# Kernel optimization log

Measured on AMD Instinct MI355X. Metric: run time of the kernel, lower is better.

The kernel has to match this reference:

```python
import jax, jax.numpy as jnp
import numpy as np

L, B, D = 2048, 8, 768
EPS_BN = 1e-5
EPS_LN = 1e-5
SCALE = 1.0 / float(np.sqrt(D))


def setup_inputs() -> dict:
    key = jax.random.key(0)
    ks = jax.random.split(key, 8)
    f32 = jnp.float32
    return {
        "x_a": jax.random.normal(ks[0], (L, B, D), dtype=f32),
        "x_v": jax.random.normal(ks[1], (L, B, D), dtype=f32),
        "x": jax.random.normal(ks[2], (L, B, D), dtype=f32),
        # conv1x1 (audio branch): weight [out_ch, in_ch], bias [out_ch]
        "W_a": jax.random.normal(ks[3], (D, D), dtype=f32) * 0.02,
        "b_a": jnp.zeros((D,), f32),
        "bn_a_g": jnp.ones((D,), f32),
        "bn_a_b": jnp.zeros((D,), f32),
        "prelu_a": jnp.full((1,), 0.25, f32),
        # conv1x1 (video branch)
        "W_v": jax.random.normal(ks[4], (D, D), dtype=f32) * 0.02,
        "b_v": jnp.zeros((D,), f32),
        "bn_v_g": jnp.ones((D,), f32),
        "bn_v_b": jnp.zeros((D,), f32),
        "prelu_v": jnp.full((1,), 0.25, f32),
        # final LayerNorm affine
        "ln_g": jnp.ones((D,), f32),
        "ln_b": jnp.zeros((D,), f32),
    }


def _branch(q, kv, W, b, bn_g, bn_b, alpha):
    # q: [B, L, D] queries; kv: [B, Lm, D] keys == values (cross-modal)
    attn = jax.nn.softmax(jnp.einsum('bld,bmd->blm', q, kv) * SCALE, axis=-1)
    ctx = jnp.einsum('blm,bmd->bld', attn, kv)            # [B, L, D]
    # Conv1d(kernel=1) over channel dim D == per-position linear
    y = jnp.einsum('bld,ed->ble', ctx, W) + b             # [B, L, D]
    # BatchNorm1d in training mode: batch stats over (B, L) per channel, biased var
    mean = jnp.mean(y, axis=(0, 1))
    var = jnp.var(y, axis=(0, 1))
    y = (y - mean) * jax.lax.rsqrt(var + EPS_BN) * bn_g + bn_b
    # PReLU (single shared alpha)
    return jnp.where(y > 0, y, alpha * y)


def reference(x_a, x_v, x, W_a, b_a, bn_a_g, bn_a_b, prelu_a,
              W_v, b_v, bn_v_g, bn_v_b, prelu_v, ln_g, ln_b):
    xa = jnp.swapaxes(x_a, 0, 1)   # [B, La, D]
    xv = jnp.swapaxes(x_v, 0, 1)   # [B, Lv, D]
    xq = jnp.swapaxes(x, 0, 1)     # [B, L, D]

    res_a = _branch(xq, xa, W_a, b_a, bn_a_g, bn_a_b, prelu_a)
    res_v = _branch(xq, xv, W_v, b_v, bn_v_g, bn_v_b, prelu_v)

    out = xq + res_a + res_v
    out = jnp.swapaxes(out, 0, 1)  # back to [L, B, D]

    mu = jnp.mean(out, axis=-1, keepdims=True)
    var = jnp.var(out, axis=-1, keepdims=True)
    return (out - mu) * jax.lax.rsqrt(var + EPS_LN) * ln_g + ln_b
```

## Files before the change

kernel.cpp:

```cpp
#include <hip/hip_runtime.h>
#include <stdint.h>

#define LL 2048
#define BB 8
#define DD 768
#define NROWS (LL*BB)
#define QKSCALE 0.03608439182435161f
#define EP 72

typedef __attribute__((ext_vector_type(8))) short short8;
typedef __attribute__((ext_vector_type(4))) float f32x4;
typedef unsigned short u16;
typedef unsigned int u32;

__device__ __forceinline__ float bf2f(u16 u) {
    union { u32 u; float f; } c; c.u = ((u32)u) << 16; return c.f;
}
__device__ __forceinline__ u16 f2bf(float f) {
    union { float f; u32 u; } c; c.f = f;
    return (u16)((c.u + 0x8000u) >> 16);
}

__global__ __launch_bounds__(256)
void cvt_kernel(const float* __restrict__ s0, u16* __restrict__ d0,
                const float* __restrict__ s1, u16* __restrict__ d1,
                const float* __restrict__ s2, u16* __restrict__ d2,
                const float* __restrict__ s3, u16* __restrict__ d3,
                const float* __restrict__ s4, u16* __restrict__ d4,
                int nbig4, int nsmall4)
{
    const float* src; u16* dst; int n4;
    switch (blockIdx.y) {
        case 0: src = s0; dst = d0; n4 = nbig4; break;
        case 1: src = s1; dst = d1; n4 = nbig4; break;
        case 2: src = s2; dst = d2; n4 = nbig4; break;
        case 3: src = s3; dst = d3; n4 = nsmall4; break;
        default: src = s4; dst = d4; n4 = nsmall4; break;
    }
    for (int i = blockIdx.x * 256 + threadIdx.x; i < n4; i += gridDim.x * 256) {
        float4 v = *(const float4*)&src[i * 4];
        ushort4 o;
        o.x = f2bf(v.x); o.y = f2bf(v.y); o.z = f2bf(v.z); o.w = f2bf(v.w);
        *(ushort4*)&dst[i * 4] = o;
    }
}

__device__ __forceinline__ void gll16(const u16* g, u16* l) {
    __builtin_amdgcn_global_load_lds((const __attribute__((address_space(1))) u32*)g,
                                     (__attribute__((address_space(3))) u32*)l, 16, 0, 0);
}

template<int EPI>
__global__ __launch_bounds__(512, 2)
void gemm_bt256(const u16* __restrict__ A, int lda, long astr,
                const u16* __restrict__ B, int ldb, long bstr,
                u16* __restrict__ C, long cstr, int ldc,
                int K, int sw,
                float* __restrict__ lsum,
                const float* __restrict__ bias,
                float* __restrict__ stats)
{
    __shared__ u16 lds[65536];

    const int tid = threadIdx.x;
    const int z = blockIdx.z;
    const int flat = blockIdx.y * gridDim.x + blockIdx.x;
    const int per = sw * gridDim.x;
    const int bm = (flat / per) * sw + (flat % sw);
    const int bn = (flat % per) / sw;
    const int m0 = bm * 256, n0 = bn * 256;

    const u16* Ab = A + (size_t)z * astr + (size_t)m0 * lda;
    const u16* Bb = B + (size_t)z * bstr + (size_t)n0 * ldb;
    u16* Cb = C + (size_t)z * cstr;

    const int lane = tid & 63, w = tid >> 6;
    const int wm = w >> 2, wn = w & 3;
    const int lr = lane & 15, lg = lane >> 4;

    const int tr = tid >> 3;
    const int sg = (tid & 7) ^ ((tid >> 3) & 7);
    const u16* pA = Ab + (size_t)tr * lda + sg * 8;
    const u16* pB = Bb + (size_t)tr * ldb + sg * 8;
    const size_t lda64 = (size_t)64 * lda;
    const size_t ldb64 = (size_t)64 * ldb;

    const int sl0 = (lg) ^ (lr & 7);
    const int sl1 = (4 + lg) ^ (lr & 7);
    const int aro = wm * 128 + lr;
    const int bro = wn * 64 + lr;
    const int aof0 = aro * 64 + sl0 * 8;
    const int aof1 = aro * 64 + sl1 * 8;
    const int bof0 = 16384 + bro * 64 + sl0 * 8;
    const int bof1 = 16384 + bro * 64 + sl1 * 8;

    f32x4 acc[8][4];
    const f32x4 zz = {0.f, 0.f, 0.f, 0.f};
    #pragma unroll
    for (int i = 0; i < 8; ++i)
        #pragma unroll
        for (int j = 0; j < 4; ++j) acc[i][j] = zz;

    const int nt = K >> 6;

    short8 af[4][2], b01[2][2], b23[2][2];

    gll16(pA,             lds + tid * 8);
    gll16(pA + lda64,     lds + 4096 + tid * 8);
    gll16(pA + 2 * lda64, lds + 8192 + tid * 8);
    gll16(pA + 3 * lda64, lds + 12288 + tid * 8);
    gll16(pB,             lds + 16384 + tid * 8);
    gll16(pB + ldb64,     lds + 20480 + tid * 8);
    gll16(pB + 2 * ldb64, lds + 24576 + tid * 8);
    gll16(pB + 3 * ldb64, lds + 28672 + tid * 8);
    gll16(pB + 64,             lds + 32768 + 16384 + tid * 8);
    gll16(pB + 64 + ldb64,     lds + 32768 + 20480 + tid * 8);
    gll16(pB + 64 + 2 * ldb64, lds + 32768 + 24576 + tid * 8);
    gll16(pB + 64 + 3 * ldb64, lds + 32768 + 28672 + tid * 8);
    asm volatile("s_waitcnt vmcnt(4)" ::: "memory");
    asm volatile("s_barrier" ::: "memory");

#define LGKM0()  do { asm volatile("s_waitcnt lgkmcnt(0)" ::: "memory"); \
                      __builtin_amdgcn_sched_barrier(0); } while (0)
#define BARR()   asm volatile("s_barrier" ::: "memory")

#define TILE(T, DB, STA, STB, VM)                                                       \
    {                                                                                   \
        const int T_ = (T);                                                             \
        const u16* sA = pA + (size_t)(T_ + 1) * 64;                                     \
        const u16* sB = pB + (size_t)(T_ + 2) * 64;                                     \
        const int DBX = (DB) ^ 32768;                                                   \
            \
        _Pragma("unroll")                                                               \
        for (int mi = 0; mi < 4; ++mi) {                                                \
            af[mi][0] = *(const short8*)&lds[(DB) + aof0 + mi * 1024];                  \
            af[mi][1] = *(const short8*)&lds[(DB) + aof1 + mi * 1024];                  \
        }                                                                               \
        _Pragma("unroll")                                                               \
        for (int ni = 0; ni < 2; ++ni) {                                                \
            b01[ni][0] = *(const short8*)&lds[(DB) + bof0 + ni * 1024];                 \
            b01[ni][1] = *(const short8*)&lds[(DB) + bof1 + ni * 1024];                 \
        }                                                                               \
        if (STA) { gll16(sA, lds + DBX + tid * 8);                                      \
                   gll16(sA + lda64, lds + DBX + 4096 + tid * 8); }                     \
        BARR();                                                                         \
        LGKM0();                                                                        \
        __builtin_amdgcn_s_setprio(1);                                                  \
        _Pragma("unroll")                                                               \
        for (int mi = 0; mi < 4; ++mi)                                                  \
            _Pragma("unroll")                                                           \
            for (int ni = 0; ni < 2; ++ni) {                                            \
                acc[mi][ni] = __builtin_amdgcn_mfma_f32_16x16x32_bf16(af[mi][0], b01[ni][0], acc[mi][ni], 0, 0, 0); \
                acc[mi][ni] = __builtin_amdgcn_mfma_f32_16x16x32_bf16(af[mi][1], b01[ni][1], acc[mi][ni], 0, 0, 0); \
            }                                                                           \
        __builtin_amdgcn_s_setprio(0);                                                  \
        BARR();                                                                         \
                                   \
        _Pragma("unroll")                                                               \
        for (int ni = 0; ni < 2; ++ni) {                                                \
            b23[ni][0] = *(const short8*)&lds[(DB) + bof0 + 2048 + ni * 1024];          \
            b23[ni][1] = *(const short8*)&lds[(DB) + bof1 + 2048 + ni * 1024];          \
        }                                                                               \
        if (STA) { gll16(sA + 2 * lda64, lds + DBX + 8192 + tid * 8);                   \
                   gll16(sA + 3 * lda64, lds + DBX + 12288 + tid * 8); }                \
        BARR();                                                                         \
        LGKM0();                                                                        \
        __builtin_amdgcn_s_setprio(1);                                                  \
        _Pragma("unroll")                                                               \
        for (int mi = 0; mi < 4; ++mi)                                                  \
            _Pragma("unroll")                                                           \
            for (int ni = 0; ni < 2; ++ni) {                                            \
                acc[mi][ni + 2] = __builtin_amdgcn_mfma_f32_16x16x32_bf16(af[mi][0], b23[ni][0], acc[mi][ni + 2], 0, 0, 0); \
                acc[mi][ni + 2] = __builtin_amdgcn_mfma_f32_16x16x32_bf16(af[mi][1], b23[ni][1], acc[mi][ni + 2], 0, 0, 0); \
            }                                                                           \
        __builtin_amdgcn_s_setprio(0);                                                  \
        BARR();                                                                         \
                       \
        _Pragma("unroll")                                                               \
        for (int mi = 0; mi < 4; ++mi) {                                                \
            af[mi][0] = *(const short8*)&lds[(DB) + aof0 + 4096 + mi * 1024];           \
            af[mi][1] = *(const short8*)&lds[(DB) + aof1 + 4096 + mi * 1024];           \
        }                                                                               \
        if (STB) { gll16(sB, lds + (DB) + 16384 + tid * 8);                             \
                   gll16(sB + ldb64, lds + (DB) + 20480 + tid * 8); }                   \
        BARR();                                                                         \
        LGKM0();                                                                        \
        __builtin_amdgcn_s_setprio(1);                                                  \
        _Pragma("unroll")                                                               \
        for (int mi = 0; mi < 4; ++mi)                                                  \
            _Pragma("unroll")                                                           \
            for (int ni = 0; ni < 2; ++ni) {                                            \
                acc[mi + 4][ni] = __builtin_amdgcn_mfma_f32_16x16x32_bf16(af[mi][0], b01[ni][0], acc[mi + 4][ni], 0, 0, 0); \
                acc[mi + 4][ni] = __builtin_amdgcn_mfma_f32_16x16x32_bf16(af[mi][1], b01[ni][1], acc[mi + 4][ni], 0, 0, 0); \
            }                                                                           \
        __builtin_amdgcn_s_setprio(0);                                                  \
        BARR();                                                                         \
         \
        if (STB) { gll16(sB + 2 * ldb64, lds + (DB) + 24576 + tid * 8);                 \
                   gll16(sB + 3 * ldb64, lds + (DB) + 28672 + tid * 8); }               \
        if ((VM) == 4)      { asm volatile("s_waitcnt vmcnt(4)" ::: "memory"); }        \
        else if ((VM) == 0) { asm volatile("s_waitcnt vmcnt(0)" ::: "memory"); }        \
        BARR();                                                                         \
        __builtin_amdgcn_s_setprio(1);                                                  \
        _Pragma("unroll")                                                               \
        for (int mi = 0; mi < 4; ++mi)                                                  \
            _Pragma("unroll")                                                           \
            for (int ni = 0; ni < 2; ++ni) {                                            \
                acc[mi + 4][ni + 2] = __builtin_amdgcn_mfma_f32_16x16x32_bf16(af[mi][0], b23[ni][0], acc[mi + 4][ni + 2], 0, 0, 0); \
                acc[mi + 4][ni + 2] = __builtin_amdgcn_mfma_f32_16x16x32_bf16(af[mi][1], b23[ni][1], acc[mi + 4][ni + 2], 0, 0, 0); \
            }                                                                           \
        __builtin_amdgcn_s_setprio(0);                                                  \
        BARR();                                                                         \
    }

    for (int t = 0; t + 2 < nt; t += 2) {
        TILE(t, 0, 1, 1, 4)
        TILE(t + 1, 32768, 1, 1, 4)
    }
    TILE(nt - 2, 0, 1, 0, 0)
    TILE(nt - 1, 32768, 0, 0, -1)
#undef TILE
#undef LGKM0
#undef BARR

    u16* eb = lds + w * 4608;

    float invl[8][4]; float bcol[4];
    if constexpr (EPI == 2) {
        #pragma unroll
        for (int mi = 0; mi < 8; ++mi)
            #pragma unroll
            for (int r = 0; r < 4; ++r)
                invl[mi][r] = 1.0f / lsum[z * 2048 + m0 + wm * 128 + mi * 16 + lg * 4 + r];
        #pragma unroll
        for (int ni = 0; ni < 4; ++ni)
            bcol[ni] = bias[n0 + wn * 64 + ni * 16 + lr];
    }
    float csum[4] = {0, 0, 0, 0}, csq[4] = {0, 0, 0, 0};

    #pragma unroll
    for (int half = 0; half < 2; ++half) {
        #pragma unroll
        for (int mi = 0; mi < 4; ++mi) {
            const int MI = half * 4 + mi;
            float rsum[4] = {0, 0, 0, 0};
            #pragma unroll
            for (int ni = 0; ni < 4; ++ni) {
                #pragma unroll
                for (int r = 0; r < 4; ++r) {
                    float v = acc[MI][ni][r];
                    if constexpr (EPI == 1) { v = __expf(v * QKSCALE); rsum[r] += v; }
                    if constexpr (EPI == 2) { v = v * invl[MI][r] + bcol[ni]; csum[ni] += v; csq[ni] += v * v; }
                    eb[(mi * 16 + lg * 4 + r) * EP + ni * 16 + lr] = f2bf(v);
                }
            }
            if constexpr (EPI == 1) {
                #pragma unroll
                for (int r = 0; r < 4; ++r) {
                    float s = rsum[r];
                    s += __shfl_xor(s, 1); s += __shfl_xor(s, 2);
                    s += __shfl_xor(s, 4); s += __shfl_xor(s, 8);
                    if (lr == 0)
                        atomicAdd(&lsum[z * 2048 + m0 + wm * 128 + MI * 16 + lg * 4 + r], s);
                }
            }
        }
        #pragma unroll
        for (int c = 0; c < 8; ++c) {
            int row = c * 8 + (lane >> 3);
            short8 v = *(const short8*)&eb[row * EP + (lane & 7) * 8];
            *(short8*)&Cb[(size_t)(m0 + wm * 128 + half * 64 + row) * ldc + n0 + wn * 64 + (lane & 7) * 8] = v;
        }
    }
    if constexpr (EPI == 2) {
        #pragma unroll
        for (int ni = 0; ni < 4; ++ni) {
            float s = csum[ni], q = csq[ni];
            s += __shfl_xor(s, 16); s += __shfl_xor(s, 32);
            q += __shfl_xor(q, 16); q += __shfl_xor(q, 32);
            if (lg == 0) {
                atomicAdd(&stats[n0 + wn * 64 + ni * 16 + lr], s);
                atomicAdd(&stats[DD + n0 + wn * 64 + ni * 16 + lr], q);
            }
        }
    }
}

__global__ void bn_params(const float* __restrict__ stats_a, const float* __restrict__ stats_v,
                          const float* __restrict__ g_a, const float* __restrict__ be_a,
                          const float* __restrict__ g_v, const float* __restrict__ be_v,
                          float* __restrict__ bnp_a, float* __restrict__ bnp_v)
{
    const int e = threadIdx.x;
    const float* st = (blockIdx.x == 0) ? stats_a : stats_v;
    const float* g  = (blockIdx.x == 0) ? g_a  : g_v;
    const float* be = (blockIdx.x == 0) ? be_a : be_v;
    float* bnp = (blockIdx.x == 0) ? bnp_a : bnp_v;
    float mean = st[e] * (1.0f / NROWS);
    float var  = st[DD + e] * (1.0f / NROWS) - mean * mean;
    float scale = g[e] * rsqrtf(var + 1e-5f);
    bnp[e]      = scale;
    bnp[DD + e] = be[e] - mean * scale;
}

__global__ __launch_bounds__(256)
void final_kernel(const float* __restrict__ x,
                  const u16* __restrict__ y_a, const u16* __restrict__ y_v,
                  const float* __restrict__ bnp_a, const float* __restrict__ bnp_v,
                  const float* __restrict__ pra, const float* __restrict__ prv,
                  const float* __restrict__ lng, const float* __restrict__ lnb,
                  float* __restrict__ out)
{
    const int n = blockIdx.x;
    const int tid = threadIdx.x;
    __shared__ float vrow[DD];
    __shared__ float reds[4], reds2[4];
    const float aa = pra[0];
    const float av = prv[0];
    const size_t base = (size_t)n * DD;
    float s = 0.f, s2 = 0.f;
    for (int e = tid; e < DD; e += 256) {
        float ya = bf2f(y_a[base + e]) * bnp_a[e] + bnp_a[DD + e];
        ya = ya > 0.f ? ya : aa * ya;
        float yv = bf2f(y_v[base + e]) * bnp_v[e] + bnp_v[DD + e];
        yv = yv > 0.f ? yv : av * yv;
        float v = x[base + e] + ya + yv;
        vrow[e] = v;
        s += v; s2 += v * v;
    }
    for (int off = 32; off > 0; off >>= 1) { s += __shfl_xor(s, off); s2 += __shfl_xor(s2, off); }
    const int wv = tid >> 6;
    if ((tid & 63) == 0) { reds[wv] = s; reds2[wv] = s2; }
    __syncthreads();
    float ts  = reds[0] + reds[1] + reds[2] + reds[3];
    float ts2 = reds2[0] + reds2[1] + reds2[2] + reds2[3];
    float mean = ts * (1.0f / DD);
    float var  = ts2 * (1.0f / DD) - mean * mean;
    float rstd = rsqrtf(var + 1e-5f);
    for (int e = tid; e < DD; e += 256) {
        float o = (vrow[e] - mean) * rstd * lng[e] + lnb[e];
        out[base + e] = o;
    }
}

extern "C" void kernel_launch(void* const* d_in, const int* in_sizes, int n_in,
                              void* d_out, int out_size, void* d_ws, size_t ws_size,
                              hipStream_t stream)
{
    const float* x_a    = (const float*)d_in[0];
    const float* x_v    = (const float*)d_in[1];
    const float* x      = (const float*)d_in[2];
    const float* W_a    = (const float*)d_in[3];
    const float* b_a    = (const float*)d_in[4];
    const float* bn_a_g = (const float*)d_in[5];
    const float* bn_a_b = (const float*)d_in[6];
    const float* pr_a   = (const float*)d_in[7];
    const float* W_v    = (const float*)d_in[8];
    const float* b_v    = (const float*)d_in[9];
    const float* bn_v_g = (const float*)d_in[10];
    const float* bn_v_b = (const float*)d_in[11];
    const float* pr_v   = (const float*)d_in[12];
    const float* ln_g   = (const float*)d_in[13];
    const float* ln_b   = (const float*)d_in[14];

    float* stats_a = (float*)d_ws;
    float* stats_v = stats_a + 1536;
    float* bnp_a   = stats_v + 1536;
    float* bnp_v   = bnp_a + 1536;
    float* lsum    = bnp_v + 1536;
    u16* xq_bf = (u16*)(lsum + 16 * 2048);
    u16* xa_bf = xq_bf + (size_t)NROWS * DD;
    u16* xv_bf = xa_bf + (size_t)NROWS * DD;
    u16* Wa_bf = xv_bf + (size_t)NROWS * DD;
    u16* Wv_bf = Wa_bf + (size_t)DD * DD;
    u16* UT    = Wv_bf + (size_t)DD * DD;
    u16* y_a = xa_bf;
    u16* y_v = xv_bf;
    size_t fixed_bytes = (size_t)((char*)UT - (char*)d_ws);

    int nb = 1;
    for (int cand = 8; cand >= 1; cand >>= 1) {
        size_t need = fixed_bytes + (size_t)cand * (3145728ull + 8388608ull);
        if (need <= ws_size) { nb = cand; break; }
    }
    u16* P = UT + (size_t)nb * (768 * 2048);

    hipMemsetAsync(stats_a, 0, (4 * 1536 + 16 * 2048) * sizeof(float), stream);

    cvt_kernel<<<dim3(3072, 5), 256, 0, stream>>>(
        x, xq_bf, x_a, xa_bf, x_v, xv_bf, W_a, Wa_bf, W_v, Wv_bf,
        NROWS * DD / 4, DD * DD / 4);

    const u16*   KVs[2]   = { xa_bf, xv_bf };
    const u16*   Ws[2]    = { Wa_bf, Wv_bf };
    const float* BIs[2]   = { b_a, b_v };
    u16*         Ys[2]    = { y_a, y_v };
    float*       STs[2]   = { stats_a, stats_v };

    for (int br = 0; br < 2; ++br) {
        const u16* kv = KVs[br];
        for (int c0 = 0; c0 < 8; c0 += nb) {
            float* lsum_bc = (nb == 8) ? (lsum + br * 8 * 2048) : lsum;
            if (nb != 8)
                hipMemsetAsync(lsum, 0, (size_t)nb * 2048 * sizeof(float), stream);
            gemm_bt256<0><<<dim3(8, 3, nb), 512, 0, stream>>>(
                Ws[br], DD, 0, kv + c0 * DD, BB * DD, DD,
                UT, (long)768 * 2048, 2048, DD, 3, nullptr, nullptr, nullptr);
            gemm_bt256<1><<<dim3(8, 8, nb), 512, 0, stream>>>(
                xq_bf + c0 * DD, BB * DD, DD, kv + c0 * DD, BB * DD, DD,
                P, (long)2048 * 2048, 2048, DD, 4, lsum_bc, nullptr, nullptr);
            gemm_bt256<2><<<dim3(3, 8, nb), 512, 0, stream>>>(
                P, 2048, (long)2048 * 2048, UT, 2048, (long)768 * 2048,
                Ys[br] + (size_t)c0 * DD, DD, BB * DD, 2048, 4, lsum_bc, BIs[br], STs[br]);
        }
    }

    bn_params<<<2, 768, 0, stream>>>(stats_a, stats_v, bn_a_g, bn_a_b, bn_v_g, bn_v_b, bnp_a, bnp_v);
    final_kernel<<<NROWS, 256, 0, stream>>>(x, y_a, y_v, bnp_a, bnp_v, pr_a, pr_v, ln_g, ln_b,
                                            (float*)d_out);
}
```

Baseline: 531.8 us.

## Batch both attention branches into single GEMM launches and remap workgroups across XCDs

Each GEMM kernel gains alternate A/B/C/bias/stats pointers selected by blockIdx.z>=8, so both branches run in one launch per stage with a 16-deep z grid when workspace allows. Workgroup IDs are also remapped so consecutive tiles spread across XCD groups, changing cache locality. The aim is fewer launches and better GPU fill and tail behavior, at the cost of a larger workspace requirement; otherwise it falls back to the per-branch loop.

```diff
diff --git a/kernel.cpp b/kernel.cpp
--- a/kernel.cpp
+++ b/kernel.cpp
@@ -52,27 +52,33 @@
 
 template<int EPI>
 __global__ __launch_bounds__(512, 2)
-void gemm_bt256(const u16* __restrict__ A, int lda, long astr,
-                const u16* __restrict__ B, int ldb, long bstr,
-                u16* __restrict__ C, long cstr, int ldc,
+void gemm_bt256(const u16* __restrict__ A, const u16* __restrict__ Aalt, int lda, long astr,
+                const u16* __restrict__ B, const u16* __restrict__ Balt, int ldb, long bstr,
+                u16* __restrict__ C, u16* __restrict__ Calt, long cstr, int ldc,
                 int K, int sw,
                 float* __restrict__ lsum,
-                const float* __restrict__ bias,
-                float* __restrict__ stats)
+                const float* __restrict__ bias, const float* __restrict__ biasAlt,
+                float* __restrict__ stats, float* __restrict__ statsAlt)
 {
     __shared__ u16 lds[65536];
 
     const int tid = threadIdx.x;
     const int z = blockIdx.z;
-    const int flat = blockIdx.y * gridDim.x + blockIdx.x;
+    const int zl = z & 7;
+    const bool hi = z >= 8;
+
+    const int lid = blockIdx.y * gridDim.x + blockIdx.x;
+    const int nwg = gridDim.x * gridDim.y;
+    const int q = nwg >> 3;
+    const int rid = (lid & 7) * q + (lid >> 3);
     const int per = sw * gridDim.x;
-    const int bm = (flat / per) * sw + (flat % sw);
-    const int bn = (flat % per) / sw;
+    const int bm = (rid / per) * sw + (rid % sw);
+    const int bn = (rid % per) / sw;
     const int m0 = bm * 256, n0 = bn * 256;
 
-    const u16* Ab = A + (size_t)z * astr + (size_t)m0 * lda;
-    const u16* Bb = B + (size_t)z * bstr + (size_t)n0 * ldb;
-    u16* Cb = C + (size_t)z * cstr;
+    const u16* Ab = (hi ? Aalt : A) + (size_t)zl * astr + (size_t)m0 * lda;
+    const u16* Bb = (hi ? Balt : B) + (size_t)zl * bstr + (size_t)n0 * ldb;
+    u16* Cb = (hi ? Calt : C) + (size_t)zl * cstr;
 
     const int lane = tid & 63, w = tid >> 6;
     const int wm = w >> 2, wn = w & 3;
@@ -225,6 +231,9 @@
 
     u16* eb = lds + w * 4608;
 
+    const float* biasP = hi ? biasAlt : bias;
+    float* statsP = hi ? statsAlt : stats;
+
     float invl[8][4]; float bcol[4];
     if constexpr (EPI == 2) {
         #pragma unroll
@@ -234,7 +243,7 @@
                 invl[mi][r] = 1.0f / lsum[z * 2048 + m0 + wm * 128 + mi * 16 + lg * 4 + r];
         #pragma unroll
         for (int ni = 0; ni < 4; ++ni)
-            bcol[ni] = bias[n0 + wn * 64 + ni * 16 + lr];
+            bcol[ni] = biasP[n0 + wn * 64 + ni * 16 + lr];
     }
     float csum[4] = {0, 0, 0, 0}, csq[4] = {0, 0, 0, 0};
 
@@ -275,12 +284,12 @@
     if constexpr (EPI == 2) {
         #pragma unroll
         for (int ni = 0; ni < 4; ++ni) {
-            float s = csum[ni], q = csq[ni];
+            float s = csum[ni], q2 = csq[ni];
             s += __shfl_xor(s, 16); s += __shfl_xor(s, 32);
-            q += __shfl_xor(q, 16); q += __shfl_xor(q, 32);
+            q2 += __shfl_xor(q2, 16); q2 += __shfl_xor(q2, 32);
             if (lg == 0) {
-                atomicAdd(&stats[n0 + wn * 64 + ni * 16 + lr], s);
-                atomicAdd(&stats[DD + n0 + wn * 64 + ni * 16 + lr], q);
+                atomicAdd(&statsP[n0 + wn * 64 + ni * 16 + lr], s);
+                atomicAdd(&statsP[DD + n0 + wn * 64 + ni * 16 + lr], q2);
             }
         }
     }
@@ -378,12 +387,8 @@
     u16* y_v = xv_bf;
     size_t fixed_bytes = (size_t)((char*)UT - (char*)d_ws);
 
-    int nb = 1;
-    for (int cand = 8; cand >= 1; cand >>= 1) {
-        size_t need = fixed_bytes + (size_t)cand * (3145728ull + 8388608ull);
-        if (need <= ws_size) { nb = cand; break; }
-    }
-    u16* P = UT + (size_t)nb * (768 * 2048);
+    const size_t UTS = (size_t)768 * 2048;
+    const size_t PS  = (size_t)2048 * 2048;
 
     hipMemsetAsync(stats_a, 0, (4 * 1536 + 16 * 2048) * sizeof(float), stream);
 
@@ -391,27 +396,59 @@
         x, xq_bf, x_a, xa_bf, x_v, xv_bf, W_a, Wa_bf, W_v, Wv_bf,
         NROWS * DD / 4, DD * DD / 4);
 
-    const u16*   KVs[2]   = { xa_bf, xv_bf };
-    const u16*   Ws[2]    = { Wa_bf, Wv_bf };
-    const float* BIs[2]   = { b_a, b_v };
-    u16*         Ys[2]    = { y_a, y_v };
-    float*       STs[2]   = { stats_a, stats_v };
-
-    for (int br = 0; br < 2; ++br) {
-        const u16* kv = KVs[br];
-        for (int c0 = 0; c0 < 8; c0 += nb) {
-            float* lsum_bc = (nb == 8) ? (lsum + br * 8 * 2048) : lsum;
-            if (nb != 8)
-                hipMemsetAsync(lsum, 0, (size_t)nb * 2048 * sizeof(float), stream);
-            gemm_bt256<0><<<dim3(8, 3, nb), 512, 0, stream>>>(
-                Ws[br], DD, 0, kv + c0 * DD, BB * DD, DD,
-                UT, (long)768 * 2048, 2048, DD, 3, nullptr, nullptr, nullptr);
-            gemm_bt256<1><<<dim3(8, 8, nb), 512, 0, stream>>>(
-                xq_bf + c0 * DD, BB * DD, DD, kv + c0 * DD, BB * DD, DD,
-                P, (long)2048 * 2048, 2048, DD, 4, lsum_bc, nullptr, nullptr);
-            gemm_bt256<2><<<dim3(3, 8, nb), 512, 0, stream>>>(
-                P, 2048, (long)2048 * 2048, UT, 2048, (long)768 * 2048,
-                Ys[br] + (size_t)c0 * DD, DD, BB * DD, 2048, 4, lsum_bc, BIs[br], STs[br]);
+    bool fused = fixed_bytes + 16ull * (UTS + PS) * 2ull <= ws_size;
+
+    if (fused) {
+        u16* P = UT + 16 * UTS;
+        gemm_bt256<0><<<dim3(8, 3, 16), 512, 0, stream>>>(
+            Wa_bf, Wv_bf, DD, 0,
+            xa_bf, xv_bf, BB * DD, DD,
+            UT, UT + 8 * UTS, (long)UTS, 2048, DD, 3,
+            nullptr, nullptr, nullptr, nullptr, nullptr);
+        gemm_bt256<1><<<dim3(8, 8, 16), 512, 0, stream>>>(
+            xq_bf, xq_bf, BB * DD, DD,
+            xa_bf, xv_bf, BB * DD, DD,
+            P, P + 8 * PS, (long)PS, 2048, DD, 4,
+            lsum, nullptr, nullptr, nullptr, nullptr);
+        gemm_bt256<2><<<dim3(3, 8, 16), 512, 0, stream>>>(
+            P, P + 8 * PS, 2048, (long)PS,
+            UT, UT + 8 * UTS, 2048, (long)UTS,
+            y_a, y_v, DD, BB * DD, 2048, 4,
+            lsum, b_a, b_v, stats_a, stats_v);
+    } else {
+        int nb = 1;
+        for (int cand = 8; cand >= 1; cand >>= 1) {
+            size_t need = fixed_bytes + (size_t)cand * (UTS + PS) * 2ull;
+            if (need <= ws_size) { nb = cand; break; }
+        }
+        u16* P = UT + (size_t)nb * UTS;
+
+        const u16*   KVs[2]   = { xa_bf, xv_bf };
+        const u16*   Ws[2]    = { Wa_bf, Wv_bf };
+        const float* BIs[2]   = { b_a, b_v };
+        u16*         Ys[2]    = { y_a, y_v };
+        float*       STs[2]   = { stats_a, stats_v };
+
+        for (int br = 0; br < 2; ++br) {
+            const u16* kv = KVs[br];
+            for (int c0 = 0; c0 < 8; c0 += nb) {
+                float* lsum_bc = (nb == 8) ? (lsum + br * 8 * 2048) : lsum;
+                if (nb != 8)
+                    hipMemsetAsync(lsum, 0, (size_t)nb * 2048 * sizeof(float), stream);
+                gemm_bt256<0><<<dim3(8, 3, nb), 512, 0, stream>>>(
+                    Ws[br], Ws[br], DD, 0, kv + c0 * DD, kv + c0 * DD, BB * DD, DD,
+                    UT, UT, (long)UTS, 2048, DD, 3,
+                    nullptr, nullptr, nullptr, nullptr, nullptr);
+                gemm_bt256<1><<<dim3(8, 8, nb), 512, 0, stream>>>(
+                    xq_bf + c0 * DD, xq_bf + c0 * DD, BB * DD, DD,
+                    kv + c0 * DD, kv + c0 * DD, BB * DD, DD,
+                    P, P, (long)PS, 2048, DD, 4,
+                    lsum_bc, nullptr, nullptr, nullptr, nullptr);
+                gemm_bt256<2><<<dim3(3, 8, nb), 512, 0, stream>>>(
+                    P, P, 2048, (long)PS, UT, UT, 2048, (long)UTS,
+                    Ys[br] + (size_t)c0 * DD, Ys[br] + (size_t)c0 * DD, DD, BB * DD, 2048, 4,
+                    lsum_bc, BIs[br], BIs[br], STs[br], STs[br]);
+            }
         }
     }
 
```

New measurement: 531.5 us. Within noise of the previous version (-0.1%).
